# Kernel optimization log

Measured on AMD Instinct MI355X. Metric: run time of the kernel, lower is better.

## Reference

```python
import jax, jax.numpy as jnp
import numpy as np

N, D_IN, D_OUT = 10000, 256, 256


def setup_inputs() -> dict:
    key = jax.random.key(0)
    k1, k2, k3, k4 = jax.random.split(key, 4)
    # xavier_uniform with gain=1.414 (as in the torch module)
    def xavier(k, shape, gain=1.414):
        fan_in, fan_out = shape[0], shape[1]
        bound = gain * np.sqrt(6.0 / (fan_in + fan_out))
        return jax.random.uniform(k, shape, jnp.float32, -bound, bound)
    return {
        "input": jax.random.normal(k1, (N, D_IN), jnp.float32),
        "adj": jax.random.randint(k2, (N, N), 0, 2, jnp.int32),  # binary dense adjacency
        "M": N,
        "W": xavier(k3, (D_IN, D_OUT)),
        "b": jnp.zeros((D_OUT,), jnp.float32),
        "a": xavier(k4, (D_OUT, 1)),
    }


def reference(input, adj, M, W, b, a):
    # h = tanh(X W + b); values used for attention logits
    h = jnp.tanh(input @ W + b)          # [N, F]
    inp = input @ W                      # [N, F] (values to aggregate)
    e = (h @ a)[:, 0]                    # [N] per-node logit
    # original also drops neighbors whose h row sums to exactly 0
    valid = (jnp.sum(h, axis=1) != 0)    # [N]
    mask = (adj[:M] > 0) & valid[None, :]  # [M, N]
    neg = jnp.asarray(-1e30, h.dtype)
    scores = jnp.where(mask, e[None, :], neg)           # [M, N]
    m = jnp.max(scores, axis=1, keepdims=True)
    w = jnp.where(mask, jnp.exp(scores - m), 0.0)       # masked exp
    denom = jnp.sum(w, axis=1, keepdims=True)
    att = w / jnp.maximum(denom, 1e-30)  # rows with no neighbors -> all zeros (matches torch zeros init)
    # dropout is identity in eval mode (training=False)
    return att @ inp                     # [M, F]
```

## Files before the change

kernel.cpp:

```cpp
#include <hip/hip_runtime.h>
#include <hip/hip_bf16.h>
#include <cstdint>
#include <cstddef>

#define NN      10000
#define DD      256
#define KSTEP64 157
#define MB2     79
#define KSPLIT  6

typedef __bf16 bf16x8 __attribute__((ext_vector_type(8)));
typedef float  f32x4  __attribute__((ext_vector_type(4)));

#define XG_OFF   0ull
#define XG_SIZE  (32ull * 10000 * 16)
#define WG_OFF   (XG_OFF + XG_SIZE)
#define WG_SIZE  (32ull * 256 * 16)
#define INP_OFF  (WG_OFF + WG_SIZE)
#define INP_SIZE (10000ull * 256 * 4)
#define E_OFF    (INP_OFF + INP_SIZE)
#define E_SIZE   (10016ull * 4)
#define HS_OFF   (E_OFF + E_SIZE)
#define HS_SIZE  (10016ull * 4)
#define G_OFF    (HS_OFF + HS_SIZE)
#define G_SIZE   (10016ull * 4)
#define YG_OFF   (G_OFF + G_SIZE + 256ull)
#define YG_SIZE  (316ull * 1088 * 16)
#define PN_OFF   (YG_OFF + YG_SIZE)
#define PN_SIZE  ((size_t)KSPLIT * 10000 * 272 * 4)

__device__ __forceinline__ void gl_lds16(const void* g, void* lds) {
    __builtin_amdgcn_global_load_lds(
        (const __attribute__((address_space(1))) unsigned int*)g,
        (__attribute__((address_space(3))) unsigned int*)lds,
        16, 0, 0);
}

__global__ __launch_bounds__(256) void k_build_xg(const float* __restrict__ X,
                                                  bf16x8* __restrict__ XG) {
    int idx = blockIdx.x * 256 + threadIdx.x;
    int row = idx >> 5;
    int q   = idx & 31;
    const float* src = X + row * 256 + q * 8;
    bf16x8 v;
#pragma unroll
    for (int j = 0; j < 8; ++j) v[j] = (__bf16)src[j];
    XG[q * 10000 + row] = v;
}

__global__ __launch_bounds__(256) void k_build_wg(const float* __restrict__ W,
                                                  bf16x8* __restrict__ WG) {
    int e = blockIdx.x * 256 + threadIdx.x;
    int q = e >> 8;
    int n = e & 255;
    bf16x8 v;
#pragma unroll
    for (int j = 0; j < 8; ++j) v[j] = (__bf16)W[(q * 8 + j) * 256 + n];
    WG[e] = v;
}

__global__ __launch_bounds__(256) void k_gemm1(const bf16x8* __restrict__ XG,
                                               const bf16x8* __restrict__ WG,
                                               const float* __restrict__ bvec,
                                               const float* __restrict__ avec,
                                               float* __restrict__ inp,
                                               float* __restrict__ evec,
                                               float* __restrict__ hsumv) {
    __shared__ bf16x8 Ash[320];
    __shared__ bf16x8 Bsh[1024];
    __shared__ float ePart[4][80];
    __shared__ float hPart[4][80];
    int tid = threadIdx.x, wid = tid >> 6, lane = tid & 63;
    int l15 = lane & 15, l4 = lane >> 4;
    int mb = blockIdx.x;

    f32x4 acc[4][5];
#pragma unroll
    for (int c = 0; c < 4; ++c)
#pragma unroll
        for (int rt = 0; rt < 5; ++rt) acc[c][rt] = f32x4{0.f, 0.f, 0.f, 0.f};

    for (int kb = 0; kb < 8; ++kb) {
        for (int rr = wid; rr < 5; rr += 4) {
            int c = rr * 64 + lane;
            int g = c / 80, r = c - g * 80;
            gl_lds16(XG + ((kb * 4 + g) * 10000 + mb * 80 + r), (char*)Ash + rr * 1024);
        }
        for (int rr = wid; rr < 16; rr += 4)
            gl_lds16(WG + kb * 1024 + rr * 64 + lane, (char*)Bsh + rr * 1024);
        __syncthreads();

        bf16x8 af[5];
#pragma unroll
        for (int rt = 0; rt < 5; ++rt) af[rt] = Ash[l4 * 80 + rt * 16 + l15];
#pragma unroll
        for (int c = 0; c < 4; ++c) {
            bf16x8 bf = Bsh[l4 * 256 + (wid * 4 + c) * 16 + l15];
#pragma unroll
            for (int rt = 0; rt < 5; ++rt)
                acc[c][rt] = __builtin_amdgcn_mfma_f32_16x16x32_bf16(af[rt], bf, acc[c][rt], 0, 0, 0);
        }
        __syncthreads();
    }

    float pe[5][4], ph[5][4];
#pragma unroll
    for (int rt = 0; rt < 5; ++rt)
#pragma unroll
        for (int rg = 0; rg < 4; ++rg) { pe[rt][rg] = 0.f; ph[rt][rg] = 0.f; }

#pragma unroll
    for (int c = 0; c < 4; ++c) {
        int col = (wid * 4 + c) * 16 + l15;
        float av = avec[col];
        float bv = bvec[col];
#pragma unroll
        for (int rt = 0; rt < 5; ++rt) {
#pragma unroll
            for (int rg = 0; rg < 4; ++rg) {
                int row = mb * 80 + rt * 16 + l4 * 4 + rg;
                float v = acc[c][rt][rg];
                inp[row * 256 + col] = v;
                float h = tanhf(v + bv);
                pe[rt][rg] += h * av;
                ph[rt][rg] += h;
            }
        }
    }
#pragma unroll
    for (int rt = 0; rt < 5; ++rt) {
#pragma unroll
        for (int rg = 0; rg < 4; ++rg) {
            float se = pe[rt][rg], sh = ph[rt][rg];
#pragma unroll
            for (int m = 1; m < 16; m <<= 1) {
                se += __shfl_xor(se, m);
                sh += __shfl_xor(sh, m);
            }
            if (l15 == 0) {
                int lr = rt * 16 + l4 * 4 + rg;
                ePart[wid][lr] = se;
                hPart[wid][lr] = sh;
            }
        }
    }
    __syncthreads();
    if (tid < 80) {
        float e = ePart[0][tid] + ePart[1][tid] + ePart[2][tid] + ePart[3][tid];
        float h = hPart[0][tid] + hPart[1][tid] + hPart[2][tid] + hPart[3][tid];
        evec[mb * 80 + tid] = e;
        hsumv[mb * 80 + tid] = h;
    }
}

__global__ __launch_bounds__(1024) void k_softmax_g(const float* __restrict__ evec,
                                                    const float* __restrict__ hsumv,
                                                    float* __restrict__ gv) {
    __shared__ float red[1024];
    int tid = threadIdx.x;
    float m = -3.0e38f;
    for (int i = tid; i < NN; i += 1024)
        if (hsumv[i] != 0.0f) m = fmaxf(m, evec[i]);
    red[tid] = m;
    __syncthreads();
    for (int s = 512; s > 0; s >>= 1) {
        if (tid < s) red[tid] = fmaxf(red[tid], red[tid + s]);
        __syncthreads();
    }
    float gmax = red[0];
    if (gmax < -1.0e37f) gmax = 0.0f;
    for (int i = tid; i < 10016; i += 1024) {
        float g = 0.0f;
        if (i < NN && hsumv[i] != 0.0f) g = expf(evec[i] - gmax);
        gv[i] = g;
    }
}

__global__ __launch_bounds__(256) void k_build_yg(const float* __restrict__ inp,
                                                  const float* __restrict__ gv,
                                                  bf16x8* __restrict__ YG) {
    int kb = blockIdx.x;
    for (int c = threadIdx.x; c < 1088; c += 256) {
        int gq = c / 272, n = c - gq * 272;
        int k0 = kb * 32 + gq * 8;
        bf16x8 v;
#pragma unroll
        for (int j = 0; j < 8; ++j) {
            int k = k0 + j;
            float val = 0.0f;
            if (k < NN) {
                float gk = gv[k];
                if (n < 256) val = gk * inp[k * 256 + n];
                else if (n == 256) val = gk;
            }
            v[j] = (__bf16)val;
        }
        YG[kb * 1088 + c] = v;
    }
}

__device__ __forceinline__ bf16x8 cvt_adj(int4 a, int4 b) {
    union { bf16x8 v; unsigned int u[4]; } r;
    r.u[0] = (a.x > 0 ? 0x3F80u : 0u) | (a.y > 0 ? 0x3F800000u : 0u);
    r.u[1] = (a.z > 0 ? 0x3F80u : 0u) | (a.w > 0 ? 0x3F800000u : 0u);
    r.u[2] = (b.x > 0 ? 0x3F80u : 0u) | (b.y > 0 ? 0x3F800000u : 0u);
    r.u[3] = (b.z > 0 ? 0x3F80u : 0u) | (b.w > 0 ? 0x3F800000u : 0u);
    return r.v;
}

__global__ __launch_bounds__(256, 2) void k_attn_gemm(const int* __restrict__ adj,
                                                      const bf16x8* __restrict__ YG,
                                                      float* __restrict__ pnum) {
    __shared__ bf16x8 Bsh[2][2176];
    int tid = threadIdx.x, wid = tid >> 6, lane = tid & 63;
    int l15 = lane & 15, l4 = lane >> 4;
    int bid = blockIdx.x;
    int mb = bid / KSPLIT, kc = bid % KSPLIT;
    int s0 = (kc * KSTEP64) / KSPLIT, s1 = ((kc + 1) * KSTEP64) / KSPLIT;

    int mrow = mb * 128 + wid * 32 + l15;
    const int* pA = adj + (size_t)min(mrow, NN - 1) * 10000;
    const int* pB = adj + (size_t)min(mrow + 16, NN - 1) * 10000;
    int kgrp = l4 * 8;

    f32x4 acc[2][17];
#pragma unroll
    for (int t = 0; t < 2; ++t)
#pragma unroll
        for (int ct = 0; ct < 17; ++ct) acc[t][ct] = f32x4{0.f, 0.f, 0.f, 0.f};

    int4 aA[8], aB[8];

    auto stageB = [&](int sTile, int bufIdx) {
        const bf16x8* src = YG + (size_t)sTile * 2176;
        char* dst = (char*)&Bsh[bufIdx][0];
#pragma unroll
        for (int i = 0; i < 9; ++i) {
            int rr = wid + i * 4;
            if (rr < 34) gl_lds16(src + rr * 64 + lane, dst + rr * 1024);
        }
    };
    auto loadA = [&](int sTile, int4* dstA) {
        int kk0 = min(sTile * 64 + kgrp, 9992);
        int kk1 = min(sTile * 64 + 32 + kgrp, 9992);
        const int4* qa0 = (const int4*)(pA + kk0);
        const int4* qb0 = (const int4*)(pB + kk0);
        const int4* qa1 = (const int4*)(pA + kk1);
        const int4* qb1 = (const int4*)(pB + kk1);
        dstA[0] = qa0[0]; dstA[1] = qa0[1]; dstA[2] = qb0[0]; dstA[3] = qb0[1];
        dstA[4] = qa1[0]; dstA[5] = qa1[1]; dstA[6] = qb1[0]; dstA[7] = qb1[1];
    };
    auto compute = [&](const int4* aCur, int bufIdx) {
        bf16x8 f00 = cvt_adj(aCur[0], aCur[1]);
        bf16x8 f01 = cvt_adj(aCur[2], aCur[3]);
        bf16x8 f10 = cvt_adj(aCur[4], aCur[5]);
        bf16x8 f11 = cvt_adj(aCur[6], aCur[7]);
#pragma unroll
        for (int ct = 0; ct < 17; ++ct) {
            bf16x8 fb0 = Bsh[bufIdx][l4 * 272 + ct * 16 + l15];
            acc[0][ct] = __builtin_amdgcn_mfma_f32_16x16x32_bf16(f00, fb0, acc[0][ct], 0, 0, 0);
            acc[1][ct] = __builtin_amdgcn_mfma_f32_16x16x32_bf16(f01, fb0, acc[1][ct], 0, 0, 0);
            bf16x8 fb1 = Bsh[bufIdx][1088 + l4 * 272 + ct * 16 + l15];
            acc[0][ct] = __builtin_amdgcn_mfma_f32_16x16x32_bf16(f10, fb1, acc[0][ct], 0, 0, 0);
            acc[1][ct] = __builtin_amdgcn_mfma_f32_16x16x32_bf16(f11, fb1, acc[1][ct], 0, 0, 0);
        }
    };

    stageB(s0, 0);
    __builtin_amdgcn_sched_barrier(0);
    loadA(s0, aA);
    asm volatile("s_waitcnt vmcnt(8)" ::: "memory");
    __builtin_amdgcn_s_barrier();

    int s = s0, buf = 0;
    while (s + 2 <= s1) {
        stageB(s + 1, buf ^ 1);
        __builtin_amdgcn_sched_barrier(0);
        loadA(s + 1, aB);
        __builtin_amdgcn_sched_barrier(0);
        compute(aA, buf);
        asm volatile("s_waitcnt vmcnt(8)" ::: "memory");
        __builtin_amdgcn_s_barrier();
        buf ^= 1; ++s;

        stageB(s + 1, buf ^ 1);
        __builtin_amdgcn_sched_barrier(0);
        loadA(s + 1, aA);
        __builtin_amdgcn_sched_barrier(0);
        compute(aB, buf);
        asm volatile("s_waitcnt vmcnt(8)" ::: "memory");
        __builtin_amdgcn_s_barrier();
        buf ^= 1; ++s;
    }
    if (s < s1) {
        stageB(s1, buf ^ 1);
        __builtin_amdgcn_sched_barrier(0);
        loadA(s1, aB);
        __builtin_amdgcn_sched_barrier(0);
        compute(aA, buf);
    }

    float* base = pnum + (size_t)kc * 10000 * 272;
    int r0 = mb * 128 + wid * 32;
#pragma unroll
    for (int t = 0; t < 2; ++t) {
#pragma unroll
        for (int ct = 0; ct < 17; ++ct) {
            int col = ct * 16 + l15;
#pragma unroll
            for (int rg = 0; rg < 4; ++rg) {
                int row = r0 + t * 16 + l4 * 4 + rg;
                if (row < NN) base[(size_t)row * 272 + col] = acc[t][ct][rg];
            }
        }
    }
}

__global__ __launch_bounds__(256) void k_finalize(const float* __restrict__ pnum,
                                                  float* __restrict__ out) {
    int idx = blockIdx.x * 256 + threadIdx.x;
    int i = idx >> 6, q = idx & 63;
    float4 sv = {0.f, 0.f, 0.f, 0.f};
    float den = 0.f;
#pragma unroll
    for (int kc = 0; kc < KSPLIT; ++kc) {
        const float* row = pnum + ((size_t)kc * 10000 + i) * 272;
        float4 v = ((const float4*)row)[q];
        sv.x += v.x; sv.y += v.y; sv.z += v.z; sv.w += v.w;
        den += row[256];
    }
    float r = 1.0f / fmaxf(den, 1e-30f);
    float4 o;
    o.x = sv.x * r; o.y = sv.y * r; o.z = sv.z * r; o.w = sv.w * r;
    ((float4*)(out + (size_t)i * 256))[q] = o;
}

extern "C" void kernel_launch(void* const* d_in, const int* in_sizes, int n_in,
                              void* d_out, int out_size, void* d_ws, size_t ws_size,
                              hipStream_t stream) {
    const float* X    = (const float*)d_in[0];
    const int*   adj  = (const int*)d_in[1];
    const float* W    = (const float*)d_in[3];
    const float* bvec = (const float*)d_in[4];
    const float* avec = (const float*)d_in[5];
    float* out = (float*)d_out;

    char* ws = (char*)d_ws;
    bf16x8* XG   = (bf16x8*)(ws + XG_OFF);
    bf16x8* WG   = (bf16x8*)(ws + WG_OFF);
    float*  inp  = (float*)(ws + INP_OFF);
    float*  evec = (float*)(ws + E_OFF);
    float*  hsv  = (float*)(ws + HS_OFF);
    float*  gv   = (float*)(ws + G_OFF);
    bf16x8* YG   = (bf16x8*)(ws + YG_OFF);
    float*  pnum = (float*)(ws + PN_OFF);

    k_build_xg<<<1250, 256, 0, stream>>>(X, XG);
    k_build_wg<<<32, 256, 0, stream>>>(W, WG);
    k_gemm1<<<125, 256, 0, stream>>>(XG, WG, bvec, avec, inp, evec, hsv);
    k_softmax_g<<<1, 1024, 0, stream>>>(evec, hsv, gv);
    k_build_yg<<<316, 256, 0, stream>>>(inp, gv, YG);
    k_attn_gemm<<<MB2 * KSPLIT, 256, 0, stream>>>(adj, YG, pnum);
    k_finalize<<<2500, 256, 0, stream>>>(pnum, out);
}
```

Measured before the change: 197.8 us.

## Use 256-row blocks, triple-buffered B pipeline, and XCD-aware block remap

```diff
diff --git a/kernel.cpp b/kernel.cpp
--- a/kernel.cpp
+++ b/kernel.cpp
@@ -6,7 +6,7 @@
 #define NN      10000
 #define DD      256
 #define KSTEP64 157
-#define MB2     79
+#define MB256   40
 #define KSPLIT  6
 
 typedef __bf16 bf16x8 __attribute__((ext_vector_type(8)));
@@ -25,7 +25,7 @@
 #define G_OFF    (HS_OFF + HS_SIZE)
 #define G_SIZE   (10016ull * 4)
 #define YG_OFF   (G_OFF + G_SIZE + 256ull)
-#define YG_SIZE  (316ull * 1088 * 16)
+#define YG_SIZE  (318ull * 1088 * 16)
 #define PN_OFF   (YG_OFF + YG_SIZE)
 #define PN_SIZE  ((size_t)KSPLIT * 10000 * 272 * 4)
 
@@ -208,17 +208,19 @@
     return r.v;
 }
 
-__global__ __launch_bounds__(256, 2) void k_attn_gemm(const int* __restrict__ adj,
+__global__ __launch_bounds__(512, 2) void k_attn_gemm(const int* __restrict__ adj,
                                                       const bf16x8* __restrict__ YG,
                                                       float* __restrict__ pnum) {
-    __shared__ bf16x8 Bsh[2][2176];
+    __shared__ bf16x8 Bsh[3][2176];
     int tid = threadIdx.x, wid = tid >> 6, lane = tid & 63;
     int l15 = lane & 15, l4 = lane >> 4;
-    int bid = blockIdx.x;
-    int mb = bid / KSPLIT, kc = bid % KSPLIT;
+
+    int phys = blockIdx.x;
+    int logical = (phys & 7) * 30 + (phys >> 3);
+    int kc = logical / MB256, mb = logical % MB256;
     int s0 = (kc * KSTEP64) / KSPLIT, s1 = ((kc + 1) * KSTEP64) / KSPLIT;
 
-    int mrow = mb * 128 + wid * 32 + l15;
+    int mrow = mb * 256 + wid * 32 + l15;
     const int* pA = adj + (size_t)min(mrow, NN - 1) * 10000;
     const int* pB = adj + (size_t)min(mrow + 16, NN - 1) * 10000;
     int kgrp = l4 * 8;
@@ -235,8 +237,8 @@
         const bf16x8* src = YG + (size_t)sTile * 2176;
         char* dst = (char*)&Bsh[bufIdx][0];
 #pragma unroll
-        for (int i = 0; i < 9; ++i) {
-            int rr = wid + i * 4;
+        for (int i = 0; i < 5; ++i) {
+            int rr = wid + i * 8;
             if (rr < 34) gl_lds16(src + rr * 64 + lane, dst + rr * 1024);
         }
     };
@@ -265,43 +267,49 @@
             acc[1][ct] = __builtin_amdgcn_mfma_f32_16x16x32_bf16(f11, fb1, acc[1][ct], 0, 0, 0);
         }
     };
+    auto endStepWait = [&]() {
+        if (wid < 2) asm volatile("s_waitcnt vmcnt(21)" ::: "memory");
+        else         asm volatile("s_waitcnt vmcnt(20)" ::: "memory");
+        __builtin_amdgcn_s_barrier();
+    };
 
     stageB(s0, 0);
+    stageB(s0 + 1, 1);
     __builtin_amdgcn_sched_barrier(0);
     loadA(s0, aA);
-    asm volatile("s_waitcnt vmcnt(8)" ::: "memory");
-    __builtin_amdgcn_s_barrier();
-
-    int s = s0, buf = 0;
+    loadA(s0 + 1, aB);
+    __builtin_amdgcn_sched_barrier(0);
+    endStepWait();
+
+    int s = s0, bc = 0;
+#define K4_BODY(ASET)                                                        \
+    {                                                                        \
+        int bs = bc + 2; if (bs >= 3) bs -= 3;                               \
+        stageB(s + 2, bs);                                                   \
+        __builtin_amdgcn_sched_barrier(0);                                   \
+        asm volatile("s_waitcnt vmcnt(12)" ::: "memory");                    \
+        __builtin_amdgcn_sched_barrier(0);                                   \
+        compute(ASET, bc);                                                   \
+        loadA(s + 2, ASET);                                                  \
+        endStepWait();                                                       \
+        ++s; ++bc; if (bc >= 3) bc -= 3;                                     \
+    }
     while (s + 2 <= s1) {
-        stageB(s + 1, buf ^ 1);
+        K4_BODY(aA)
+        K4_BODY(aB)
+    }
+    if (s < s1) {
+        int bs = bc + 2; if (bs >= 3) bs -= 3;
+        stageB(s + 2, bs);
         __builtin_amdgcn_sched_barrier(0);
-        loadA(s + 1, aB);
+        asm volatile("s_waitcnt vmcnt(12)" ::: "memory");
         __builtin_amdgcn_sched_barrier(0);
-        compute(aA, buf);
-        asm volatile("s_waitcnt vmcnt(8)" ::: "memory");
-        __builtin_amdgcn_s_barrier();
-        buf ^= 1; ++s;
-
-        stageB(s + 1, buf ^ 1);
-        __builtin_amdgcn_sched_barrier(0);
-        loadA(s + 1, aA);
-        __builtin_amdgcn_sched_barrier(0);
-        compute(aB, buf);
-        asm volatile("s_waitcnt vmcnt(8)" ::: "memory");
-        __builtin_amdgcn_s_barrier();
-        buf ^= 1; ++s;
-    }
-    if (s < s1) {
-        stageB(s1, buf ^ 1);
-        __builtin_amdgcn_sched_barrier(0);
-        loadA(s1, aB);
-        __builtin_amdgcn_sched_barrier(0);
-        compute(aA, buf);
-    }
+        compute(aA, bc);
+    }
+#undef K4_BODY
 
     float* base = pnum + (size_t)kc * 10000 * 272;
-    int r0 = mb * 128 + wid * 32;
+    int r0 = mb * 256 + wid * 32;
 #pragma unroll
     for (int t = 0; t < 2; ++t) {
 #pragma unroll
@@ -359,7 +367,7 @@
     k_build_wg<<<32, 256, 0, stream>>>(W, WG);
     k_gemm1<<<125, 256, 0, stream>>>(XG, WG, bvec, avec, inp, evec, hsv);
     k_softmax_g<<<1, 1024, 0, stream>>>(evec, hsv, gv);
-    k_build_yg<<<316, 256, 0, stream>>>(inp, gv, YG);
-    k_attn_gemm<<<MB2 * KSPLIT, 256, 0, stream>>>(adj, YG, pnum);
+    k_build_yg<<<318, 256, 0, stream>>>(inp, gv, YG);
+    k_attn_gemm<<<MB256 * KSPLIT, 512, 0, stream>>>(adj, YG, pnum);
     k_finalize<<<2500, 256, 0, stream>>>(pnum, out);
 }
```

Measured after the change: 267.3 us. 35.1% more time.

## Read B operand directly from global memory and remap blocks for XCD locality

Applied to the files above, without the earlier changes.

```diff
diff --git a/kernel.cpp b/kernel.cpp
--- a/kernel.cpp
+++ b/kernel.cpp
@@ -25,7 +25,7 @@
 #define G_OFF    (HS_OFF + HS_SIZE)
 #define G_SIZE   (10016ull * 4)
 #define YG_OFF   (G_OFF + G_SIZE + 256ull)
-#define YG_SIZE  (316ull * 1088 * 16)
+#define YG_SIZE  (318ull * 1088 * 16)
 #define PN_OFF   (YG_OFF + YG_SIZE)
 #define PN_SIZE  ((size_t)KSPLIT * 10000 * 272 * 4)
 
@@ -211,11 +211,14 @@
 __global__ __launch_bounds__(256, 2) void k_attn_gemm(const int* __restrict__ adj,
                                                       const bf16x8* __restrict__ YG,
                                                       float* __restrict__ pnum) {
-    __shared__ bf16x8 Bsh[2][2176];
     int tid = threadIdx.x, wid = tid >> 6, lane = tid & 63;
     int l15 = lane & 15, l4 = lane >> 4;
-    int bid = blockIdx.x;
-    int mb = bid / KSPLIT, kc = bid % KSPLIT;
+
+    int orig = blockIdx.x;
+    const int nwg = MB2 * KSPLIT, q = nwg >> 3, r = nwg & 7;
+    int x = orig & 7, o = orig >> 3;
+    int logical = (x < r ? x * (q + 1) : r * (q + 1) + (x - r) * q) + o;
+    int kc = logical / MB2, mb = logical % MB2;
     int s0 = (kc * KSTEP64) / KSPLIT, s1 = ((kc + 1) * KSTEP64) / KSPLIT;
 
     int mrow = mb * 128 + wid * 32 + l15;
@@ -229,75 +232,36 @@
 #pragma unroll
         for (int ct = 0; ct < 17; ++ct) acc[t][ct] = f32x4{0.f, 0.f, 0.f, 0.f};
 
-    int4 aA[8], aB[8];
-
-    auto stageB = [&](int sTile, int bufIdx) {
-        const bf16x8* src = YG + (size_t)sTile * 2176;
-        char* dst = (char*)&Bsh[bufIdx][0];
-#pragma unroll
-        for (int i = 0; i < 9; ++i) {
-            int rr = wid + i * 4;
-            if (rr < 34) gl_lds16(src + rr * 64 + lane, dst + rr * 1024);
-        }
-    };
-    auto loadA = [&](int sTile, int4* dstA) {
+    int4 aA[8];
+    auto loadA = [&](int sTile) {
         int kk0 = min(sTile * 64 + kgrp, 9992);
         int kk1 = min(sTile * 64 + 32 + kgrp, 9992);
         const int4* qa0 = (const int4*)(pA + kk0);
         const int4* qb0 = (const int4*)(pB + kk0);
         const int4* qa1 = (const int4*)(pA + kk1);
         const int4* qb1 = (const int4*)(pB + kk1);
-        dstA[0] = qa0[0]; dstA[1] = qa0[1]; dstA[2] = qb0[0]; dstA[3] = qb0[1];
-        dstA[4] = qa1[0]; dstA[5] = qa1[1]; dstA[6] = qb1[0]; dstA[7] = qb1[1];
+        aA[0] = qa0[0]; aA[1] = qa0[1]; aA[2] = qb0[0]; aA[3] = qb0[1];
+        aA[4] = qa1[0]; aA[5] = qa1[1]; aA[6] = qb1[0]; aA[7] = qb1[1];
     };
-    auto compute = [&](const int4* aCur, int bufIdx) {
-        bf16x8 f00 = cvt_adj(aCur[0], aCur[1]);
-        bf16x8 f01 = cvt_adj(aCur[2], aCur[3]);
-        bf16x8 f10 = cvt_adj(aCur[4], aCur[5]);
-        bf16x8 f11 = cvt_adj(aCur[6], aCur[7]);
+
+    loadA(s0);
+    for (int s = s0; s < s1; ++s) {
+        bf16x8 f00 = cvt_adj(aA[0], aA[1]);
+        bf16x8 f01 = cvt_adj(aA[2], aA[3]);
+        bf16x8 f10 = cvt_adj(aA[4], aA[5]);
+        bf16x8 f11 = cvt_adj(aA[6], aA[7]);
+        loadA(s + 1);
+
+        const bf16x8* bs = YG + (size_t)s * 2176 + l4 * 272 + l15;
 #pragma unroll
         for (int ct = 0; ct < 17; ++ct) {
-            bf16x8 fb0 = Bsh[bufIdx][l4 * 272 + ct * 16 + l15];
+            bf16x8 fb0 = bs[ct * 16];
+            bf16x8 fb1 = bs[1088 + ct * 16];
             acc[0][ct] = __builtin_amdgcn_mfma_f32_16x16x32_bf16(f00, fb0, acc[0][ct], 0, 0, 0);
             acc[1][ct] = __builtin_amdgcn_mfma_f32_16x16x32_bf16(f01, fb0, acc[1][ct], 0, 0, 0);
-            bf16x8 fb1 = Bsh[bufIdx][1088 + l4 * 272 + ct * 16 + l15];
             acc[0][ct] = __builtin_amdgcn_mfma_f32_16x16x32_bf16(f10, fb1, acc[0][ct], 0, 0, 0);
             acc[1][ct] = __builtin_amdgcn_mfma_f32_16x16x32_bf16(f11, fb1, acc[1][ct], 0, 0, 0);
         }
-    };
-
-    stageB(s0, 0);
-    __builtin_amdgcn_sched_barrier(0);
-    loadA(s0, aA);
-    asm volatile("s_waitcnt vmcnt(8)" ::: "memory");
-    __builtin_amdgcn_s_barrier();
-
-    int s = s0, buf = 0;
-    while (s + 2 <= s1) {
-        stageB(s + 1, buf ^ 1);
-        __builtin_amdgcn_sched_barrier(0);
-        loadA(s + 1, aB);
-        __builtin_amdgcn_sched_barrier(0);
-        compute(aA, buf);
-        asm volatile("s_waitcnt vmcnt(8)" ::: "memory");
-        __builtin_amdgcn_s_barrier();
-        buf ^= 1; ++s;
-
-        stageB(s + 1, buf ^ 1);
-        __builtin_amdgcn_sched_barrier(0);
-        loadA(s + 1, aA);
-        __builtin_amdgcn_sched_barrier(0);
-        compute(aB, buf);
-        asm volatile("s_waitcnt vmcnt(8)" ::: "memory");
-        __builtin_amdgcn_s_barrier();
-        buf ^= 1; ++s;
-    }
-    if (s < s1) {
-        stageB(s1, buf ^ 1);
-        __builtin_amdgcn_sched_barrier(0);
-        loadA(s1, aB);
-        __builtin_amdgcn_sched_barrier(0);
-        compute(aA, buf);
     }
 
     float* base = pnum + (size_t)kc * 10000 * 272;
@@ -359,7 +323,7 @@
     k_build_wg<<<32, 256, 0, stream>>>(W, WG);
     k_gemm1<<<125, 256, 0, stream>>>(XG, WG, bvec, avec, inp, evec, hsv);
     k_softmax_g<<<1, 1024, 0, stream>>>(evec, hsv, gv);
-    k_build_yg<<<316, 256, 0, stream>>>(inp, gv, YG);
+    k_build_yg<<<318, 256, 0, stream>>>(inp, gv, YG);
     k_attn_gemm<<<MB2 * KSPLIT, 256, 0, stream>>>(adj, YG, pnum);
     k_finalize<<<2500, 256, 0, stream>>>(pnum, out);
 }
```

After: 270.8 us. 1.37x slower.
